# Kernel tuning notes

Hardware: AMD Instinct MI355X
Metric: run time of the kernel (lower is better)

Reference implementation:

```python
import jax, jax.numpy as jnp
import numpy as np

# Module config (matches init_kwargs)
DIM = 1024
NUM_HEADS = 16
HEAD_DIM = DIM // NUM_HEADS
SCALE = HEAD_DIM ** -0.5
WINDOW = 256
EXT = WINDOW // 2  # overlap_window=True -> ext_size = window_size // 2

B, N = 4, 4096  # N is a multiple of WINDOW


def setup_inputs() -> dict:
    key = jax.random.key(0)
    ks = jax.random.split(key, 5)
    x = jax.random.normal(ks[0], (B, N, DIM), dtype=jnp.float32)
    # Learned params (trunc-normal std=0.02 in torch; plain normal*0.02 is fine as a stand-in)
    w_qkv = jax.random.normal(ks[1], (3 * DIM, DIM), dtype=jnp.float32) * 0.02
    b_qkv = jnp.zeros((3 * DIM,), dtype=jnp.float32)
    w_proj = jax.random.normal(ks[2], (DIM, DIM), dtype=jnp.float32) * 0.02
    b_proj = jnp.zeros((DIM,), dtype=jnp.float32)
    return {"x": x, "w_qkv": w_qkv, "b_qkv": b_qkv, "w_proj": w_proj, "b_proj": b_proj}


def _local_attention(x, w_qkv, b_qkv, w_proj, b_proj):
    b, n, c = x.shape
    h, hd, w, e = NUM_HEADS, HEAD_DIM, WINDOW, EXT
    g = n // w  # number of windows (n is a multiple of w)
    kw_len = w + 2 * e  # extended window length for keys/values

    # qkv projection and head split: (3, b, h, n, hd)
    qkv = (x @ w_qkv.T + b_qkv).reshape(b, n, 3, h, hd).transpose(2, 0, 3, 1, 4)
    q, k, v = qkv[0], qkv[1], qkv[2]

    # q: non-overlapping windows -> (b, h, g, w, hd)
    qw = q.reshape(b, h, g, w, hd)

    # k, v: pad seq by ext on both sides, then strided overlapping windows
    kp = jnp.pad(k, ((0, 0), (0, 0), (e, e), (0, 0)))
    vp = jnp.pad(v, ((0, 0), (0, 0), (e, e), (0, 0)))
    # window g covers padded positions [g*w, g*w + kw_len)
    idx = jnp.arange(g)[:, None] * w + jnp.arange(kw_len)[None, :]  # (g, kw_len)
    kw = kp[:, :, idx]  # (b, h, g, kw_len, hd)
    vw = vp[:, :, idx]

    # per-window attention
    dots = jnp.einsum('bhgqd,bhgkd->bhgqk', qw, kw) * SCALE  # (b, h, g, w, kw_len)
    # mask out keys that came from the ext padding (out of [0, n) range)
    pos = idx - e  # global key positions per window
    valid = (pos >= 0) & (pos < n)  # (g, kw_len)
    dots = jnp.where(valid[None, None, :, None, :], dots, -jnp.inf)
    attn = jax.nn.softmax(dots, axis=-1)
    out = jnp.einsum('bhgqk,bhgkd->bhgqd', attn, vw)  # (b, h, g, w, hd)

    # merge windows and heads: (b, n, c)
    out = out.reshape(b, h, n, hd).transpose(0, 2, 1, 3).reshape(b, n, c)
    return out @ w_proj.T + b_proj


def reference(x, w_qkv, b_qkv, w_proj, b_proj):
    return _local_attention(x, w_qkv, b_qkv, w_proj, b_proj)
```

## Files before the change

kernel.cpp:

```cpp
#include <hip/hip_runtime.h>


typedef __attribute__((ext_vector_type(8))) short short8;
typedef __attribute__((ext_vector_type(4))) float f32x4;
typedef __attribute__((ext_vector_type(8))) unsigned short ushort8v;
typedef __attribute__((ext_vector_type(4))) unsigned short ushort4v;
typedef __attribute__((ext_vector_type(4))) unsigned int uint4v;
typedef __attribute__((ext_vector_type(4))) _Float16 half4;

#define K_DIM 1024

__device__ __forceinline__ unsigned short f2bf(float f) {
  unsigned int u = __builtin_bit_cast(unsigned int, f);
  u += 0x7FFFu + ((u >> 16) & 1u);
  return (unsigned short)(u >> 16);
}
__device__ __forceinline__ unsigned short f2h(float f) {
  _Float16 h = (_Float16)f;
  return __builtin_bit_cast(unsigned short, h);
}
__device__ __forceinline__ void gload_lds(const unsigned short* g, unsigned short* l) {
  __builtin_amdgcn_global_load_lds((const __attribute__((address_space(1))) void*)g,
                                   (__attribute__((address_space(3))) void*)l, 16, 0, 0);
}

__global__ __launch_bounds__(256) void convf2b(const float* __restrict__ src,
                                               unsigned short* __restrict__ dst, int n4) {
  int i = blockIdx.x * blockDim.x + threadIdx.x;
  if (i >= n4) return;
  f32x4 v = *(const f32x4*)(src + (size_t)i * 4);
  ushort4v o;
  o[0] = f2bf(v[0]); o[1] = f2bf(v[1]); o[2] = f2bf(v[2]); o[3] = f2bf(v[3]);
  *(ushort4v*)(dst + (size_t)i * 4) = o;
}

__device__ __forceinline__ void gemm_core(const unsigned short* __restrict__ A,
                                          const unsigned short* __restrict__ Bw,
                                          unsigned short* As, unsigned short* Bs,
                                          int m0, int f0, int tid, f32x4 acc[4][4]) {
  const int lane = tid & 63;
  const int w = tid >> 6;
  const int wm = (tid >> 7) & 1;
  const int wn = (tid >> 6) & 1;
  const int q15 = lane & 15, quad = lane >> 4;
  const int sw = q15 & 3;
  for (int kk = 0; kk < K_DIM; kk += 32) {
#pragma unroll
    for (int r = 0; r < 2; ++r) {
      int c = tid + r * 256;
      int row = c >> 2, s = c & 3;
      int gs = s ^ (row & 3);
      const unsigned short* ga = A + (size_t)(m0 + row) * K_DIM + kk + gs * 8;
      const unsigned short* gb = Bw + (size_t)(f0 + row) * K_DIM + kk + gs * 8;
      unsigned short* la = As + (size_t)(w * 64 + r * 256) * 8;
      unsigned short* lb = Bs + (size_t)(w * 64 + r * 256) * 8;
      gload_lds(ga, la);
      gload_lds(gb, lb);
    }
    __syncthreads();
    short8 af[4], bf[4];
#pragma unroll
    for (int i = 0; i < 4; ++i)
      af[i] = *(const short8*)&As[(wm * 64 + i * 16 + q15) * 32 + (quad ^ sw) * 8];
#pragma unroll
    for (int j = 0; j < 4; ++j)
      bf[j] = *(const short8*)&Bs[(wn * 64 + j * 16 + q15) * 32 + (quad ^ sw) * 8];
#pragma unroll
    for (int i = 0; i < 4; ++i)
#pragma unroll
      for (int j = 0; j < 4; ++j)
        acc[i][j] = __builtin_amdgcn_mfma_f32_16x16x32_bf16(af[i], bf[j], acc[i][j], 0, 0, 0);
    __syncthreads();
  }
}

__global__ __launch_bounds__(256) void gemm_qkv(const unsigned short* __restrict__ A,
                                                const unsigned short* __restrict__ Bw,
                                                const float* __restrict__ bias,
                                                unsigned short* __restrict__ q,
                                                unsigned short* __restrict__ k,
                                                unsigned short* __restrict__ v) {
  __shared__ unsigned short As[128 * 32];
  __shared__ unsigned short Bs[128 * 32];
  int m0 = (blockIdx.x & 127) * 128;
  int f0 = (blockIdx.x >> 7) * 128;
  int tid = threadIdx.x;
  f32x4 acc[4][4] = {};
  gemm_core(A, Bw, As, Bs, m0, f0, tid, acc);
  int lane = tid & 63;
  int wm = (tid >> 7) & 1, wn = (tid >> 6) & 1;
  int which = f0 >> 10;
  unsigned short* dst = (which == 0) ? q : ((which == 1) ? k : v);
#pragma unroll
  for (int j = 0; j < 4; ++j) {
    int f = f0 + wn * 64 + j * 16 + (lane & 15);
    int hh = (f >> 6) & 15;
    int d = f & 63;
    float bj = bias[f];
#pragma unroll
    for (int i = 0; i < 4; ++i) {
#pragma unroll
      for (int r = 0; r < 4; ++r) {
        int m = m0 + wm * 64 + i * 16 + (lane >> 4) * 4 + r;
        int bb = m >> 12, n = m & 4095;
        float val = acc[i][j][r] + bj;
        dst[((size_t)(bb * 16 + hh) * 4096 + n) * 64 + d] =
            (which == 2) ? f2h(val) : f2bf(val);
      }
    }
  }
}

__global__ __launch_bounds__(256) void gemm_proj(const unsigned short* __restrict__ A,
                                                 const unsigned short* __restrict__ Bw,
                                                 const float* __restrict__ bias,
                                                 float* __restrict__ out) {
  __shared__ unsigned short As[128 * 32];
  __shared__ unsigned short Bs[128 * 32];
  int m0 = (blockIdx.x & 127) * 128;
  int f0 = (blockIdx.x >> 7) * 128;
  int tid = threadIdx.x;
  f32x4 acc[4][4] = {};
  gemm_core(A, Bw, As, Bs, m0, f0, tid, acc);
  int lane = tid & 63;
  int wm = (tid >> 7) & 1, wn = (tid >> 6) & 1;
#pragma unroll
  for (int j = 0; j < 4; ++j) {
    int f = f0 + wn * 64 + j * 16 + (lane & 15);
    float bj = bias[f];
#pragma unroll
    for (int i = 0; i < 4; ++i) {
#pragma unroll
      for (int r = 0; r < 4; ++r) {
        int m = m0 + wm * 64 + i * 16 + (lane >> 4) * 4 + r;
        out[(size_t)m * 1024 + f] = acc[i][j][r] + bj;
      }
    }
  }
}

__global__ __launch_bounds__(256) void transpose_v(const unsigned short* __restrict__ v,
                                                   unsigned short* __restrict__ vt) {
  __shared__ unsigned short tile[64][72];
  int bid = blockIdx.x;
  int bh = bid >> 6;
  int n0 = (bid & 63) * 64;
  int tid = threadIdx.x;
#pragma unroll
  for (int r = 0; r < 2; ++r) {
    int c = tid + r * 256;
    int row = c >> 3, col8 = (c & 7) * 8;
    uint4v dv = *(const uint4v*)&v[((size_t)bh * 4096 + n0 + row) * 64 + col8];
    *(uint4v*)&tile[row][col8] = dv;
  }
  __syncthreads();
#pragma unroll
  for (int r = 0; r < 2; ++r) {
    int c = tid + r * 256;
    int d = c >> 3, n8 = (c & 7) * 8;
    ushort8v o;
#pragma unroll
    for (int ii = 0; ii < 8; ++ii) o[ii] = tile[n8 + ii][d];
    *(ushort8v*)&vt[((size_t)bh * 64 + d) * 4096 + n0 + n8] = o;
  }
}

__global__ __launch_bounds__(256) void attn3(const unsigned short* __restrict__ Q,
                                             const unsigned short* __restrict__ Kb,
                                             const unsigned short* __restrict__ Vt,
                                             unsigned short* __restrict__ Ao) {
  __shared__ unsigned short lds2[2][8192];

  int bid = blockIdx.x;
  int qb = bid & 63;
  int bh = bid >> 6;
  int b = bh >> 4, h = bh & 15;
  int tid = threadIdx.x, lane = tid & 63, w = tid >> 6;
  int q0 = qb * 64 + w * 16;
  int g = qb >> 2;
  int kst = g * 256 - 128;
  const size_t base = (size_t)bh * 4096 * 64;
  const int q15 = lane & 15, quad = lane >> 4;

  short8 bq[2];
#pragma unroll
  for (int s = 0; s < 2; ++s)
    bq[s] = *(const short8*)&Q[base + (size_t)(q0 + q15) * 64 + s * 32 + quad * 8];

  half4 spk[32];
  float mx = -1e30f;

  auto stageK = [&](int c, int buf) {
    int kb = kst + c * 128;
    kb = min(max(kb, 0), 4096 - 128);
    const unsigned short* Kg = Kb + base + (size_t)kb * 64;
#pragma unroll
    for (int i = 0; i < 4; ++i) {
      int slot = tid + i * 256;
      int row = slot >> 3, s = slot & 7;
      int gs = s ^ (row & 7);
      gload_lds(Kg + (size_t)row * 64 + gs * 8, &lds2[buf][(w * 64 + i * 256) * 8]);
    }
  };

  stageK(0, 0);
#pragma unroll
  for (int c = 0; c < 4; ++c) {
    __syncthreads();
    if (c < 3) stageK(c + 1, (c + 1) & 1);
    const unsigned short* Kc = lds2[c & 1];
    int r7 = q15 & 7;
#pragma unroll
    for (int nt = 0; nt < 8; ++nt) {
      int t = c * 8 + nt;
      int ky = kst + c * 128 + nt * 16;
      bool valid = (ky >= 0) && (ky < 4096);
      if (valid) {
        int sg0 = quad ^ r7;
        const unsigned short* kr = &Kc[(nt * 16 + q15) * 64];
        short8 ak0 = *(const short8*)&kr[sg0 * 8];
        short8 ak1 = *(const short8*)&kr[(sg0 ^ 4) * 8];
        f32x4 sa = {0.f, 0.f, 0.f, 0.f};
        sa = __builtin_amdgcn_mfma_f32_16x16x32_bf16(ak0, bq[0], sa, 0, 0, 0);
        sa = __builtin_amdgcn_mfma_f32_16x16x32_bf16(ak1, bq[1], sa, 0, 0, 0);
        float s0 = sa[0] * 0.125f, s1 = sa[1] * 0.125f;
        float s2 = sa[2] * 0.125f, s3 = sa[3] * 0.125f;
        mx = fmaxf(mx, fmaxf(fmaxf(s0, s1), fmaxf(s2, s3)));
        half4 pk;
        pk[0] = (_Float16)s0; pk[1] = (_Float16)s1;
        pk[2] = (_Float16)s2; pk[3] = (_Float16)s3;
        spk[t] = pk;
      } else {
        spk[t] = (half4){(_Float16)0.f, (_Float16)0.f, (_Float16)0.f, (_Float16)0.f};
      }
    }
  }
  mx = fmaxf(mx, __shfl_xor(mx, 16, 64));
  mx = fmaxf(mx, __shfl_xor(mx, 32, 64));

  auto stageV = [&](int c, int buf) {
    int kb = kst + c * 128;
    kb = min(max(kb, 0), 4096 - 128);
    const unsigned short* Vg = Vt + (size_t)bh * 64 * 4096 + kb;
#pragma unroll
    for (int i = 0; i < 4; ++i) {
      int slot = tid + i * 256;
      int d = slot >> 4, s = slot & 15;
      int gs = s ^ (d & 15);
      gload_lds(Vg + (size_t)d * 4096 + gs * 8, &lds2[buf][(w * 64 + i * 256) * 8]);
    }
  };

  float sum = 0.f;
  f32x4 oacc[4];
#pragma unroll
  for (int dt = 0; dt < 4; ++dt) oacc[dt] = (f32x4){0.f, 0.f, 0.f, 0.f};

  stageV(0, 0);
#pragma unroll
  for (int c = 0; c < 4; ++c) {
    __syncthreads();
    if (c < 3) stageV(c + 1, (c + 1) & 1);
    const unsigned short* Vc = lds2[c & 1];
#pragma unroll
    for (int nt = 0; nt < 8; ++nt) {
      int t = c * 8 + nt;
      int ky = kst + c * 128 + nt * 16;
      bool valid = (ky >= 0) && (ky < 4096);
      if (!valid) continue;
      half4 sp = spk[t];
      float p0 = __expf((float)sp[0] - mx);
      float p1 = __expf((float)sp[1] - mx);
      float p2 = __expf((float)sp[2] - mx);
      float p3 = __expf((float)sp[3] - mx);
      sum += (p0 + p1) + (p2 + p3);
      half4 pk;
      pk[0] = (_Float16)p0; pk[1] = (_Float16)p1;
      pk[2] = (_Float16)p2; pk[3] = (_Float16)p3;
      int sgb = 2 * nt + (quad >> 1);
      int eo = (quad & 1) * 4;
#pragma unroll
      for (int dt = 0; dt < 4; ++dt) {
        int d = dt * 16 + q15;
        half4 bv = *(const half4*)&Vc[d * 128 + ((sgb ^ q15) * 8) + eo];
        oacc[dt] = __builtin_amdgcn_mfma_f32_16x16x16f16(pk, bv, oacc[dt], 0, 0, 0);
      }
    }
  }
  sum += __shfl_xor(sum, 16, 64);
  sum += __shfl_xor(sum, 32, 64);
  float linv = 1.0f / sum;

  float li[4];
#pragma unroll
  for (int r = 0; r < 4; ++r) li[r] = __shfl(linv, quad * 4 + r, 64);
#pragma unroll
  for (int dt = 0; dt < 4; ++dt) {
#pragma unroll
    for (int r = 0; r < 4; ++r) {
      float o = oacc[dt][r] * li[r];
      Ao[(size_t)(b * 4096 + q0 + quad * 4 + r) * 1024 + h * 64 + dt * 16 + q15] = f2bf(o);
    }
  }
}

extern "C" void kernel_launch(void* const* d_in, const int* in_sizes, int n_in,
                              void* d_out, int out_size, void* d_ws, size_t ws_size,
                              hipStream_t stream) {
  const float* x = (const float*)d_in[0];
  const float* w_qkv = (const float*)d_in[1];
  const float* b_qkv = (const float*)d_in[2];
  const float* w_proj = (const float*)d_in[3];
  const float* b_proj = (const float*)d_in[4];
  float* out = (float*)d_out;

  unsigned short* ws = (unsigned short*)d_ws;
  unsigned short* xb = ws;
  unsigned short* wqkvb = ws + 16777216;
  unsigned short* wprojb = ws + 19922944;
  unsigned short* qb = ws + 20971520;
  unsigned short* kb = ws + 37748736;
  unsigned short* vb = ws + 54525952;
  unsigned short* attnb = ws + 71303168;
  unsigned short* vtb = xb;

  convf2b<<<16384, 256, 0, stream>>>(x, xb, 16777216 / 4);
  convf2b<<<3072, 256, 0, stream>>>(w_qkv, wqkvb, 3145728 / 4);
  convf2b<<<1024, 256, 0, stream>>>(w_proj, wprojb, 1048576 / 4);
  gemm_qkv<<<128 * 24, 256, 0, stream>>>(xb, wqkvb, b_qkv, qb, kb, vb);
  transpose_v<<<4096, 256, 0, stream>>>(vb, vtb);
  attn3<<<4096, 256, 0, stream>>>(qb, kb, vtb, attnb);
  gemm_proj<<<128 * 8, 256, 0, stream>>>(attnb, wprojb, b_proj, out);
}
```

Measured before the change: 429.8 us.

## Rewrite GEMM core with 256x128 tiles and triple-buffered async LDS pipeline

Replaces the single-buffered 128x128, K=32 GEMM loop with a 256x128 tile, K=64 step, 512-thread kernel that triple-buffers global-to-LDS loads and waits with explicit vmcnt counters, so loads overlap the MFMA work. It uses an 8-way XOR swizzle, splits each K step into two halves with staged prefetch, and raises wave priority around the MFMA blocks. The aim is to hide global memory latency and remove the two full barriers per iteration in both projection GEMMs. The cost is a 144KB LDS footprint per block and hand-tuned wait counts that must match the number of issued loads exactly.

```diff
diff --git a/kernel.cpp b/kernel.cpp
--- a/kernel.cpp
+++ b/kernel.cpp
@@ -34,66 +34,159 @@
   *(ushort4v*)(dst + (size_t)i * 4) = o;
 }
 
-__device__ __forceinline__ void gemm_core(const unsigned short* __restrict__ A,
-                                          const unsigned short* __restrict__ Bw,
-                                          unsigned short* As, unsigned short* Bs,
-                                          int m0, int f0, int tid, f32x4 acc[4][4]) {
+__device__ __forceinline__ void gemm256_core(const unsigned short* __restrict__ A,
+                                             const unsigned short* __restrict__ Bw,
+                                             unsigned short* lds,
+                                             int m0, int f0, int tid, f32x4 acc[4][4]) {
   const int lane = tid & 63;
   const int w = tid >> 6;
-  const int wm = (tid >> 7) & 1;
-  const int wn = (tid >> 6) & 1;
+  const int wm = w >> 1, wn = w & 1;
   const int q15 = lane & 15, quad = lane >> 4;
-  const int sw = q15 & 3;
-  for (int kk = 0; kk < K_DIM; kk += 32) {
-#pragma unroll
-    for (int r = 0; r < 2; ++r) {
-      int c = tid + r * 256;
-      int row = c >> 2, s = c & 3;
-      int gs = s ^ (row & 3);
-      const unsigned short* ga = A + (size_t)(m0 + row) * K_DIM + kk + gs * 8;
-      const unsigned short* gb = Bw + (size_t)(f0 + row) * K_DIM + kk + gs * 8;
-      unsigned short* la = As + (size_t)(w * 64 + r * 256) * 8;
-      unsigned short* lb = Bs + (size_t)(w * 64 + r * 256) * 8;
-      gload_lds(ga, la);
-      gload_lds(gb, lb);
-    }
-    __syncthreads();
+  const int r7 = q15 & 7;
+
+  const unsigned short* Ag = A + (size_t)m0 * K_DIM;
+  const unsigned short* Bg = Bw + (size_t)f0 * K_DIM;
+
+  int arow[4], ags[4];
+#pragma unroll
+  for (int r = 0; r < 4; ++r) {
+    int slot = r * 512 + tid;
+    arow[r] = slot >> 3;
+    ags[r] = (slot & 7) ^ (arow[r] & 7);
+  }
+  int brow[2], bgs[2];
+#pragma unroll
+  for (int r = 0; r < 2; ++r) {
+    int slot = r * 512 + tid;
+    brow[r] = slot >> 3;
+    bgs[r] = (slot & 7) ^ (brow[r] & 7);
+  }
+
+  auto stageA = [&](int bufs, int kk, int r) {
+    gload_lds(Ag + (size_t)arow[r] * K_DIM + kk + ags[r] * 8,
+              lds + bufs * 24576 + (r * 512 + w * 64) * 8);
+  };
+  auto stageB = [&](int bufs, int kk, int r) {
+    gload_lds(Bg + (size_t)brow[r] * K_DIM + kk + bgs[r] * 8,
+              lds + bufs * 24576 + 16384 + (r * 512 + w * 64) * 8);
+  };
+
+#pragma unroll
+  for (int r = 0; r < 4; ++r) stageA(0, 0, r);
+#pragma unroll
+  for (int r = 0; r < 2; ++r) stageB(0, 0, r);
+#pragma unroll
+  for (int r = 0; r < 4; ++r) stageA(1, 64, r);
+#pragma unroll
+  for (int r = 0; r < 2; ++r) stageB(1, 64, r);
+
+  const int aoff0 = (wm * 64 + q15) * 8;
+  const int boff0 = (wn * 64 + q15) * 8;
+
+  int buf = 0;
+#pragma unroll 3
+  for (int t = 0; t < 15; ++t) {
+    int bufs = buf + 2; if (bufs >= 3) bufs -= 3;
+    const int kks = (t + 2) * 64;
+    const bool st = (t < 14);
+    const unsigned short* Asb = lds + buf * 24576;
+    const unsigned short* Bsb = Asb + 16384;
     short8 af[4], bf[4];
-#pragma unroll
-    for (int i = 0; i < 4; ++i)
-      af[i] = *(const short8*)&As[(wm * 64 + i * 16 + q15) * 32 + (quad ^ sw) * 8];
-#pragma unroll
-    for (int j = 0; j < 4; ++j)
-      bf[j] = *(const short8*)&Bs[(wn * 64 + j * 16 + q15) * 32 + (quad ^ sw) * 8];
+
+    asm volatile("s_waitcnt vmcnt(6)" ::: "memory");
+    __builtin_amdgcn_s_barrier();
+    __builtin_amdgcn_sched_barrier(0);
+    {
+      int sg = quad ^ r7;
+#pragma unroll
+      for (int i = 0; i < 4; ++i)
+        af[i] = *(const short8*)&Asb[(size_t)(aoff0 + i * 128 + sg) * 8];
+#pragma unroll
+      for (int j = 0; j < 4; ++j)
+        bf[j] = *(const short8*)&Bsb[(size_t)(boff0 + j * 128 + sg) * 8];
+    }
+    if (st) { stageA(bufs, kks, 0); stageA(bufs, kks, 1); stageB(bufs, kks, 0); }
+    __builtin_amdgcn_s_setprio(1);
 #pragma unroll
     for (int i = 0; i < 4; ++i)
 #pragma unroll
       for (int j = 0; j < 4; ++j)
         acc[i][j] = __builtin_amdgcn_mfma_f32_16x16x32_bf16(af[i], bf[j], acc[i][j], 0, 0, 0);
-    __syncthreads();
-  }
-}
-
-__global__ __launch_bounds__(256) void gemm_qkv(const unsigned short* __restrict__ A,
-                                                const unsigned short* __restrict__ Bw,
-                                                const float* __restrict__ bias,
-                                                unsigned short* __restrict__ q,
-                                                unsigned short* __restrict__ k,
-                                                unsigned short* __restrict__ v) {
-  __shared__ unsigned short As[128 * 32];
-  __shared__ unsigned short Bs[128 * 32];
-  int m0 = (blockIdx.x & 127) * 128;
-  int f0 = (blockIdx.x >> 7) * 128;
+    __builtin_amdgcn_s_setprio(0);
+
+    __builtin_amdgcn_s_barrier();
+    __builtin_amdgcn_sched_barrier(0);
+    {
+      int sg = (4 | quad) ^ r7;
+#pragma unroll
+      for (int i = 0; i < 4; ++i)
+        af[i] = *(const short8*)&Asb[(size_t)(aoff0 + i * 128 + sg) * 8];
+#pragma unroll
+      for (int j = 0; j < 4; ++j)
+        bf[j] = *(const short8*)&Bsb[(size_t)(boff0 + j * 128 + sg) * 8];
+    }
+    if (st) { stageA(bufs, kks, 2); stageA(bufs, kks, 3); stageB(bufs, kks, 1); }
+    __builtin_amdgcn_s_setprio(1);
+#pragma unroll
+    for (int i = 0; i < 4; ++i)
+#pragma unroll
+      for (int j = 0; j < 4; ++j)
+        acc[i][j] = __builtin_amdgcn_mfma_f32_16x16x32_bf16(af[i], bf[j], acc[i][j], 0, 0, 0);
+    __builtin_amdgcn_s_setprio(0);
+
+    buf = buf + 1; if (buf >= 3) buf -= 3;
+  }
+
+  {
+    const unsigned short* Asb = lds;
+    const unsigned short* Bsb = lds + 16384;
+    short8 af[4], bf[4];
+    asm volatile("s_waitcnt vmcnt(0)" ::: "memory");
+    __builtin_amdgcn_s_barrier();
+    __builtin_amdgcn_sched_barrier(0);
+#pragma unroll
+    for (int ks = 0; ks < 2; ++ks) {
+      int sg = (ks * 4 + quad) ^ r7;
+#pragma unroll
+      for (int i = 0; i < 4; ++i)
+        af[i] = *(const short8*)&Asb[(size_t)(aoff0 + i * 128 + sg) * 8];
+#pragma unroll
+      for (int j = 0; j < 4; ++j)
+        bf[j] = *(const short8*)&Bsb[(size_t)(boff0 + j * 128 + sg) * 8];
+      __builtin_amdgcn_s_setprio(1);
+#pragma unroll
+      for (int i = 0; i < 4; ++i)
+#pragma unroll
+        for (int j = 0; j < 4; ++j)
+          acc[i][j] = __builtin_amdgcn_mfma_f32_16x16x32_bf16(af[i], bf[j], acc[i][j], 0, 0, 0);
+      __builtin_amdgcn_s_setprio(0);
+    }
+  }
+}
+
+__global__ __launch_bounds__(512, 2) void gemm_qkv(const unsigned short* __restrict__ A,
+                                                   const unsigned short* __restrict__ Bw,
+                                                   const float* __restrict__ bias,
+                                                   unsigned short* __restrict__ q,
+                                                   unsigned short* __restrict__ k,
+                                                   unsigned short* __restrict__ v) {
+  __shared__ unsigned short lds[73728];
+  int bid = blockIdx.x;
+  int mt = bid / 24, ft = bid % 24;
+  int m0 = mt * 256, f0 = ft * 128;
   int tid = threadIdx.x;
   f32x4 acc[4][4] = {};
-  gemm_core(A, Bw, As, Bs, m0, f0, tid, acc);
+  gemm256_core(A, Bw, lds, m0, f0, tid, acc);
+
   int lane = tid & 63;
-  int wm = (tid >> 7) & 1, wn = (tid >> 6) & 1;
+  int w = tid >> 6;
+  int wm = w >> 1, wn = w & 1;
+  int q15 = lane & 15, quad = lane >> 4;
   int which = f0 >> 10;
   unsigned short* dst = (which == 0) ? q : ((which == 1) ? k : v);
 #pragma unroll
   for (int j = 0; j < 4; ++j) {
-    int f = f0 + wn * 64 + j * 16 + (lane & 15);
+    int f = f0 + wn * 64 + j * 16 + q15;
     int hh = (f >> 6) & 15;
     int d = f & 63;
     float bj = bias[f];
@@ -101,7 +194,7 @@
     for (int i = 0; i < 4; ++i) {
 #pragma unroll
       for (int r = 0; r < 4; ++r) {
-        int m = m0 + wm * 64 + i * 16 + (lane >> 4) * 4 + r;
+        int m = m0 + wm * 64 + i * 16 + quad * 4 + r;
         int bb = m >> 12, n = m & 4095;
         float val = acc[i][j][r] + bj;
         dst[((size_t)(bb * 16 + hh) * 4096 + n) * 64 + d] =
@@ -111,28 +204,31 @@
   }
 }
 
-__global__ __launch_bounds__(256) void gemm_proj(const unsigned short* __restrict__ A,
-                                                 const unsigned short* __restrict__ Bw,
-                                                 const float* __restrict__ bias,
-                                                 float* __restrict__ out) {
-  __shared__ unsigned short As[128 * 32];
-  __shared__ unsigned short Bs[128 * 32];
-  int m0 = (blockIdx.x & 127) * 128;
-  int f0 = (blockIdx.x >> 7) * 128;
+__global__ __launch_bounds__(512, 2) void gemm_proj(const unsigned short* __restrict__ A,
+                                                    const unsigned short* __restrict__ Bw,
+                                                    const float* __restrict__ bias,
+                                                    float* __restrict__ out) {
+  __shared__ unsigned short lds[73728];
+  int bid = blockIdx.x;
+  int mt = bid >> 3, ft = bid & 7;
+  int m0 = mt * 256, f0 = ft * 128;
   int tid = threadIdx.x;
   f32x4 acc[4][4] = {};
-  gemm_core(A, Bw, As, Bs, m0, f0, tid, acc);
+  gemm256_core(A, Bw, lds, m0, f0, tid, acc);
+
   int lane = tid & 63;
-  int wm = (tid >> 7) & 1, wn = (tid >> 6) & 1;
+  int w = tid >> 6;
+  int wm = w >> 1, wn = w & 1;
+  int q15 = lane & 15, quad = lane >> 4;
 #pragma unroll
   for (int j = 0; j < 4; ++j) {
-    int f = f0 + wn * 64 + j * 16 + (lane & 15);
+    int f = f0 + wn * 64 + j * 16 + q15;
     float bj = bias[f];
 #pragma unroll
     for (int i = 0; i < 4; ++i) {
 #pragma unroll
       for (int r = 0; r < 4; ++r) {
-        int m = m0 + wm * 64 + i * 16 + (lane >> 4) * 4 + r;
+        int m = m0 + wm * 64 + i * 16 + quad * 4 + r;
         out[(size_t)m * 1024 + f] = acc[i][j][r] + bj;
       }
     }
@@ -327,8 +423,8 @@
   convf2b<<<16384, 256, 0, stream>>>(x, xb, 16777216 / 4);
   convf2b<<<3072, 256, 0, stream>>>(w_qkv, wqkvb, 3145728 / 4);
   convf2b<<<1024, 256, 0, stream>>>(w_proj, wprojb, 1048576 / 4);
-  gemm_qkv<<<128 * 24, 256, 0, stream>>>(xb, wqkvb, b_qkv, qb, kb, vb);
+  gemm_qkv<<<64 * 24, 512, 0, stream>>>(xb, wqkvb, b_qkv, qb, kb, vb);
   transpose_v<<<4096, 256, 0, stream>>>(vb, vtb);
   attn3<<<4096, 256, 0, stream>>>(qb, kb, vtb, attnb);
-  gemm_proj<<<128 * 8, 256, 0, stream>>>(attnb, wprojb, b_proj, out);
-}
+  gemm_proj<<<64 * 8, 512, 0, stream>>>(attnb, wprojb, b_proj, out);
+}
```

Result: faster. 403.8 us (-6.1%).

## Use 256x256 double-buffered GEMM tiles with 512 threads for projections

Applied to the files above, without the earlier changes.

Replaces the 128x128, BK=32 single-buffered GEMM core with a 256x256 tile, BK=64, double-buffered LDS pipeline run by 8 waves. The next k-slice is prefetched with global_load_lds while MFMAs consume the current one, there is one barrier per iteration, and s_setprio is raised around the MFMA block. The goal is higher arithmetic intensity and overlap of global loads with compute in the QKV and output projections. The 128 KB of LDS and large accumulator arrays limit occupancy, and gemm_proj now launches only 256 blocks, which may underfill the GPU.

```diff
diff --git a/kernel.cpp b/kernel.cpp
--- a/kernel.cpp
+++ b/kernel.cpp
@@ -34,74 +34,101 @@
   *(ushort4v*)(dst + (size_t)i * 4) = o;
 }
 
-__device__ __forceinline__ void gemm_core(const unsigned short* __restrict__ A,
-                                          const unsigned short* __restrict__ Bw,
-                                          unsigned short* As, unsigned short* Bs,
-                                          int m0, int f0, int tid, f32x4 acc[4][4]) {
+__device__ __forceinline__ void gemm256_core(const unsigned short* __restrict__ A,
+                                             const unsigned short* __restrict__ Bw,
+                                             unsigned short* lds,
+                                             int m0, int f0, int tid, f32x4 acc[8][4]) {
   const int lane = tid & 63;
   const int w = tid >> 6;
-  const int wm = (tid >> 7) & 1;
-  const int wn = (tid >> 6) & 1;
+  const int wm = w >> 2, wn = w & 3;
   const int q15 = lane & 15, quad = lane >> 4;
-  const int sw = q15 & 3;
-  for (int kk = 0; kk < K_DIM; kk += 32) {
-#pragma unroll
-    for (int r = 0; r < 2; ++r) {
-      int c = tid + r * 256;
-      int row = c >> 2, s = c & 3;
-      int gs = s ^ (row & 3);
-      const unsigned short* ga = A + (size_t)(m0 + row) * K_DIM + kk + gs * 8;
-      const unsigned short* gb = Bw + (size_t)(f0 + row) * K_DIM + kk + gs * 8;
-      unsigned short* la = As + (size_t)(w * 64 + r * 256) * 8;
-      unsigned short* lb = Bs + (size_t)(w * 64 + r * 256) * 8;
-      gload_lds(ga, la);
-      gload_lds(gb, lb);
-    }
-    __syncthreads();
-    short8 af[4], bf[4];
-#pragma unroll
-    for (int i = 0; i < 4; ++i)
-      af[i] = *(const short8*)&As[(wm * 64 + i * 16 + q15) * 32 + (quad ^ sw) * 8];
-#pragma unroll
-    for (int j = 0; j < 4; ++j)
-      bf[j] = *(const short8*)&Bs[(wn * 64 + j * 16 + q15) * 32 + (quad ^ sw) * 8];
-#pragma unroll
-    for (int i = 0; i < 4; ++i)
+  const int r7 = q15 & 7;
+
+  const unsigned short* Ag = A + (size_t)m0 * K_DIM;
+  const unsigned short* Bg = Bw + (size_t)f0 * K_DIM;
+
+  int goff[4];
+#pragma unroll
+  for (int r = 0; r < 4; ++r) {
+    int slot = r * 512 + tid;
+    int row = slot >> 3, s = slot & 7;
+    goff[r] = row * K_DIM + (s ^ (row & 7)) * 8;
+  }
+
+  auto stage = [&](int bb, int kk) {
+#pragma unroll
+    for (int r = 0; r < 4; ++r)
+      gload_lds(Ag + goff[r] + kk, lds + bb * 32768 + (r * 512 + w * 64) * 8);
+#pragma unroll
+    for (int r = 0; r < 4; ++r)
+      gload_lds(Bg + goff[r] + kk, lds + bb * 32768 + 16384 + (r * 512 + w * 64) * 8);
+  };
+
+  stage(0, 0);
+
+  const int abase = (wm * 128 + q15) * 64;
+  const int bbase = 16384 + (wn * 64 + q15) * 64;
+
+#pragma unroll 2
+  for (int t = 0; t < 16; ++t) {
+    const int buf = t & 1;
+    const unsigned short* Lb = lds + buf * 32768;
+    asm volatile("s_waitcnt vmcnt(0)" ::: "memory");
+    __builtin_amdgcn_s_barrier();
+    __builtin_amdgcn_sched_barrier(0);
+    if (t < 15) stage(buf ^ 1, (t + 1) * 64);
+#pragma unroll
+    for (int ks = 0; ks < 2; ++ks) {
+      const int sg = (ks * 4 + quad) ^ r7;
+      short8 af[8], bf[4];
 #pragma unroll
       for (int j = 0; j < 4; ++j)
-        acc[i][j] = __builtin_amdgcn_mfma_f32_16x16x32_bf16(af[i], bf[j], acc[i][j], 0, 0, 0);
-    __syncthreads();
-  }
-}
-
-__global__ __launch_bounds__(256) void gemm_qkv(const unsigned short* __restrict__ A,
-                                                const unsigned short* __restrict__ Bw,
-                                                const float* __restrict__ bias,
-                                                unsigned short* __restrict__ q,
-                                                unsigned short* __restrict__ k,
-                                                unsigned short* __restrict__ v) {
-  __shared__ unsigned short As[128 * 32];
-  __shared__ unsigned short Bs[128 * 32];
-  int m0 = (blockIdx.x & 127) * 128;
-  int f0 = (blockIdx.x >> 7) * 128;
+        bf[j] = *(const short8*)&Lb[bbase + j * 1024 + sg * 8];
+#pragma unroll
+      for (int i = 0; i < 8; ++i)
+        af[i] = *(const short8*)&Lb[abase + i * 1024 + sg * 8];
+      __builtin_amdgcn_s_setprio(1);
+#pragma unroll
+      for (int i = 0; i < 8; ++i)
+#pragma unroll
+        for (int j = 0; j < 4; ++j)
+          acc[i][j] = __builtin_amdgcn_mfma_f32_16x16x32_bf16(af[i], bf[j], acc[i][j], 0, 0, 0);
+      __builtin_amdgcn_s_setprio(0);
+    }
+  }
+}
+
+__global__ __launch_bounds__(512, 2) void gemm_qkv(const unsigned short* __restrict__ A,
+                                                   const unsigned short* __restrict__ Bw,
+                                                   const float* __restrict__ bias,
+                                                   unsigned short* __restrict__ q,
+                                                   unsigned short* __restrict__ k,
+                                                   unsigned short* __restrict__ v) {
+  __shared__ unsigned short lds[65536];
+  int bid = blockIdx.x;
+  int mt = bid / 12, ft = bid % 12;
+  int m0 = mt * 256, f0 = ft * 256;
   int tid = threadIdx.x;
-  f32x4 acc[4][4] = {};
-  gemm_core(A, Bw, As, Bs, m0, f0, tid, acc);
+  f32x4 acc[8][4] = {};
+  gemm256_core(A, Bw, lds, m0, f0, tid, acc);
+
   int lane = tid & 63;
-  int wm = (tid >> 7) & 1, wn = (tid >> 6) & 1;
+  int w = tid >> 6;
+  int wm = w >> 2, wn = w & 3;
+  int q15 = lane & 15, quad = lane >> 4;
   int which = f0 >> 10;
   unsigned short* dst = (which == 0) ? q : ((which == 1) ? k : v);
 #pragma unroll
   for (int j = 0; j < 4; ++j) {
-    int f = f0 + wn * 64 + j * 16 + (lane & 15);
+    int f = f0 + wn * 64 + j * 16 + q15;
     int hh = (f >> 6) & 15;
     int d = f & 63;
     float bj = bias[f];
 #pragma unroll
-    for (int i = 0; i < 4; ++i) {
+    for (int i = 0; i < 8; ++i) {
 #pragma unroll
       for (int r = 0; r < 4; ++r) {
-        int m = m0 + wm * 64 + i * 16 + (lane >> 4) * 4 + r;
+        int m = m0 + wm * 128 + i * 16 + quad * 4 + r;
         int bb = m >> 12, n = m & 4095;
         float val = acc[i][j][r] + bj;
         dst[((size_t)(bb * 16 + hh) * 4096 + n) * 64 + d] =
@@ -111,28 +138,31 @@
   }
 }
 
-__global__ __launch_bounds__(256) void gemm_proj(const unsigned short* __restrict__ A,
-                                                 const unsigned short* __restrict__ Bw,
-                                                 const float* __restrict__ bias,
-                                                 float* __restrict__ out) {
-  __shared__ unsigned short As[128 * 32];
-  __shared__ unsigned short Bs[128 * 32];
-  int m0 = (blockIdx.x & 127) * 128;
-  int f0 = (blockIdx.x >> 7) * 128;
+__global__ __launch_bounds__(512, 2) void gemm_proj(const unsigned short* __restrict__ A,
+                                                    const unsigned short* __restrict__ Bw,
+                                                    const float* __restrict__ bias,
+                                                    float* __restrict__ out) {
+  __shared__ unsigned short lds[65536];
+  int bid = blockIdx.x;
+  int mt = bid >> 2, ft = bid & 3;
+  int m0 = mt * 256, f0 = ft * 256;
   int tid = threadIdx.x;
-  f32x4 acc[4][4] = {};
-  gemm_core(A, Bw, As, Bs, m0, f0, tid, acc);
+  f32x4 acc[8][4] = {};
+  gemm256_core(A, Bw, lds, m0, f0, tid, acc);
+
   int lane = tid & 63;
-  int wm = (tid >> 7) & 1, wn = (tid >> 6) & 1;
+  int w = tid >> 6;
+  int wm = w >> 2, wn = w & 3;
+  int q15 = lane & 15, quad = lane >> 4;
 #pragma unroll
   for (int j = 0; j < 4; ++j) {
-    int f = f0 + wn * 64 + j * 16 + (lane & 15);
+    int f = f0 + wn * 64 + j * 16 + q15;
     float bj = bias[f];
 #pragma unroll
-    for (int i = 0; i < 4; ++i) {
+    for (int i = 0; i < 8; ++i) {
 #pragma unroll
       for (int r = 0; r < 4; ++r) {
-        int m = m0 + wm * 64 + i * 16 + (lane >> 4) * 4 + r;
+        int m = m0 + wm * 128 + i * 16 + quad * 4 + r;
         out[(size_t)m * 1024 + f] = acc[i][j][r] + bj;
       }
     }
@@ -327,8 +357,8 @@
   convf2b<<<16384, 256, 0, stream>>>(x, xb, 16777216 / 4);
   convf2b<<<3072, 256, 0, stream>>>(w_qkv, wqkvb, 3145728 / 4);
   convf2b<<<1024, 256, 0, stream>>>(w_proj, wprojb, 1048576 / 4);
-  gemm_qkv<<<128 * 24, 256, 0, stream>>>(xb, wqkvb, b_qkv, qb, kb, vb);
+  gemm_qkv<<<64 * 12, 512, 0, stream>>>(xb, wqkvb, b_qkv, qb, kb, vb);
   transpose_v<<<4096, 256, 0, stream>>>(vb, vtb);
   attn3<<<4096, 256, 0, stream>>>(qb, kb, vtb, attnb);
-  gemm_proj<<<128 * 8, 256, 0, stream>>>(attnb, wprojb, b_proj, out);
-}
+  gemm_proj<<<64 * 4, 512, 0, stream>>>(attnb, wprojb, b_proj, out);
+}
```

Result: slower. 450.2 us (+4.7%).
